# Optimization experiments

Hardware: AMD Instinct MI355X
Metric: run time of the kernel (lower is better)

Reference implementation:

```python
import jax, jax.numpy as jnp
import numpy as np

DIM = 1024
DFF = 4096
LN_EPS = 1e-5


def _layernorm(x, g, b):
    mu = jnp.mean(x, axis=-1, keepdims=True)
    var = jnp.mean((x - mu) ** 2, axis=-1, keepdims=True)
    return (x - mu) * jax.lax.rsqrt(var + LN_EPS) * g + b


def setup_inputs() -> dict:
    key = jax.random.key(0)
    ks = jax.random.split(key, 16)
    B, L, D, F = 4, 2048, DIM, DFF
    return {
        "x": jax.random.normal(ks[0], (B, L, D), dtype=jnp.float32),
        "hidden_real": jax.random.normal(ks[1], (B, D), dtype=jnp.float32),
        "hidden_imag": jax.random.normal(ks[2], (B, D), dtype=jnp.float32),
        # SConvLayer params (real/imag pairs, mirroring torch.view_as_real storage)
        "phazor_init": jax.random.normal(ks[3], (D, 2), dtype=jnp.float32),
        "phazor": jax.random.normal(ks[4], (D, 2), dtype=jnp.float32),
        # fc (gate) linear
        "fc_w": jax.random.normal(ks[5], (D, D), dtype=jnp.float32) / np.sqrt(D),
        "fc_b": jax.random.normal(ks[6], (D,), dtype=jnp.float32) * 0.01,
        # FFN
        "w1": jax.random.normal(ks[7], (F, D), dtype=jnp.float32) / np.sqrt(D),
        "b1": jax.random.normal(ks[8], (F,), dtype=jnp.float32) * 0.01,
        "w2": jax.random.normal(ks[9], (D, F), dtype=jnp.float32) / np.sqrt(F),
        "b2": jax.random.normal(ks[10], (D,), dtype=jnp.float32) * 0.01,
        # shared LayerNorm (used twice in the block with the same params)
        "ln_g": jnp.ones((D,), dtype=jnp.float32),
        "ln_b": jnp.zeros((D,), dtype=jnp.float32),
    }


def reference(x, hidden_real, hidden_imag, phazor_init, phazor,
              fc_w, fc_b, w1, b1, w2, b2, ln_g, ln_b):
    B, L, D = x.shape
    hidden = (hidden_real + 1j * hidden_imag).astype(jnp.complex64)

    x_res = x
    xn = _layernorm(x, ln_g, ln_b)

    # --- SConvLayer ---
    pz = (phazor[:, 0] + 1j * phazor[:, 1]).astype(jnp.complex64)  # [D]
    # magnitude exp(-|z|^2), phase = angle(z)
    p = jnp.exp(-(pz.real ** 2 + pz.imag ** 2)) * jnp.exp(1j * jnp.angle(pz))
    t = jnp.arange(L)
    prog = p[None, :] ** t[:, None]                      # [L, D] complex
    init_c = (phazor_init[:, 0] + 1j * phazor_init[:, 1]).astype(jnp.complex64)
    filt = prog * init_c[None, :]                        # [L, D]
    n2 = 2 * L
    filt_fft = jnp.fft.fft(filt, n=n2, axis=0)           # [2L, D]
    x_fft = jnp.fft.fft(xn.astype(jnp.complex64), n=n2, axis=1)  # [B, 2L, D]
    conv = jnp.fft.ifft(filt_fft[None] * x_fft, axis=1)[:, :L]   # [B, L, D]
    conv_with_past = conv + hidden[:, None, :] * prog[None] * p[None, None, :]
    sx = conv_with_past.real

    # --- gate ---
    y = jax.nn.silu(jnp.einsum('bld,ed->ble', x_res, fc_w) + fc_b)
    x2 = sx * y + x_res

    # --- FFN (same LayerNorm params) ---
    x3 = _layernorm(x2, ln_g, ln_b)
    h = jax.nn.silu(jnp.einsum('bld,fd->blf', x3, w1) + b1)
    out = jnp.einsum('blf,df->bld', h, w2) + b2 + x2
    return out, conv_with_past
```

## Files before the change

### kernel.cpp

```cpp
#include <hip/hip_runtime.h>
#include <hip/hip_bf16.h>

#define D_MODEL 1024
#define D_FF    4096
#define SEQ_LEN 2048
#define NBATCH  4
#define NROWS   (NBATCH*SEQ_LEN)
#define NCHUNK  32
#define CHUNK_L (SEQ_LEN/NCHUNK)
#define LN_EPS  1e-5f

typedef __hip_bfloat16 bf16;
typedef __attribute__((ext_vector_type(8))) short bf16x8;
typedef __attribute__((ext_vector_type(4))) float f32x4;

__device__ __forceinline__ void gload16(const bf16* g, bf16* l) {
    __builtin_amdgcn_global_load_lds(
        (const __attribute__((address_space(1))) void*)g,
        (__attribute__((address_space(3))) void*)l, 16, 0, 0);
}

__global__ void cast4(const float4* __restrict__ in, ushort4* __restrict__ out, int n4) {
    int i = blockIdx.x * blockDim.x + threadIdx.x;
    if (i < n4) {
        float4 v = in[i];
        union { ushort4 u; bf16 b[4]; } cv;
        cv.b[0] = __float2bfloat16(v.x); cv.b[1] = __float2bfloat16(v.y);
        cv.b[2] = __float2bfloat16(v.z); cv.b[3] = __float2bfloat16(v.w);
        out[i] = cv.u;
    }
}

__global__ void compute_pvec(const float* __restrict__ phz, float* __restrict__ pv) {
    int d = blockIdx.x * blockDim.x + threadIdx.x;
    if (d >= D_MODEL) return;
    float re = phz[2*d], im = phz[2*d+1];
    float r2 = re*re + im*im;
    float mag = expf(-r2);
    float pr, pim;
    if (r2 > 0.f) { float inv = mag / sqrtf(r2); pr = re*inv; pim = im*inv; }
    else          { pr = mag; pim = 0.f; }
    float ar = pr, ai = pim;
    #pragma unroll
    for (int i = 0; i < 6; i++) { float nr = ar*ar - ai*ai; float ni = 2.f*ar*ai; ar = nr; ai = ni; }
    pv[d]            = pr;
    pv[D_MODEL+d]    = pim;
    pv[2*D_MODEL+d]  = ar;
    pv[3*D_MODEL+d]  = ai;
}

__global__ __launch_bounds__(256) void ln_fused(const float* __restrict__ x,
                                                const float* __restrict__ g,
                                                const float* __restrict__ bta,
                                                float* __restrict__ outf,
                                                bf16*  __restrict__ outb,
                                                bf16*  __restrict__ rawb)
{
    int row = blockIdx.x;
    int tid = threadIdx.x;
    const float4* xr = (const float4*)(x + (size_t)row * D_MODEL);
    float4 v = xr[tid];
    if (rawb) {
        union { ushort4 u; bf16 b[4]; } cv;
        cv.b[0]=__float2bfloat16(v.x); cv.b[1]=__float2bfloat16(v.y);
        cv.b[2]=__float2bfloat16(v.z); cv.b[3]=__float2bfloat16(v.w);
        ((ushort4*)(rawb + (size_t)row * D_MODEL))[tid] = cv.u;
    }
    float s  = v.x + v.y + v.z + v.w;
    float s2 = v.x*v.x + v.y*v.y + v.z*v.z + v.w*v.w;
    for (int off = 32; off; off >>= 1) { s += __shfl_down(s, off); s2 += __shfl_down(s2, off); }
    __shared__ float red[8];
    int wid = tid >> 6, lane = tid & 63;
    if (lane == 0) { red[wid] = s; red[4+wid] = s2; }
    __syncthreads();
    if (tid == 0) {
        red[0] = red[0]+red[1]+red[2]+red[3];
        red[4] = red[4]+red[5]+red[6]+red[7];
    }
    __syncthreads();
    float mu  = red[0] * (1.f/D_MODEL);
    float var = red[4] * (1.f/D_MODEL) - mu*mu;
    float rstd = rsqrtf(var + LN_EPS);
    float4 gv = ((const float4*)g)[tid];
    float4 bv = ((const float4*)bta)[tid];
    float4 o;
    o.x = (v.x-mu)*rstd*gv.x + bv.x;
    o.y = (v.y-mu)*rstd*gv.y + bv.y;
    o.z = (v.z-mu)*rstd*gv.z + bv.z;
    o.w = (v.w-mu)*rstd*gv.w + bv.w;
    if (outf) ((float4*)(outf + (size_t)row * D_MODEL))[tid] = o;
    if (outb) {
        union { ushort4 u; bf16 b[4]; } cv;
        cv.b[0]=__float2bfloat16(o.x); cv.b[1]=__float2bfloat16(o.y);
        cv.b[2]=__float2bfloat16(o.z); cv.b[3]=__float2bfloat16(o.w);
        ((ushort4*)(outb + (size_t)row * D_MODEL))[tid] = cv.u;
    }
}

__global__ __launch_bounds__(256) void scan_pass1(const float* __restrict__ xn,
                                                  const float* __restrict__ pv,
                                                  const float* __restrict__ pini,
                                                  float* __restrict__ Sc)
{
    int d = blockIdx.x * 256 + threadIdx.x;
    int c = blockIdx.y, b = blockIdx.z;
    float pr = pv[d], pim = pv[D_MODEL+d];
    float icr = pini[2*d], ici = pini[2*d+1];
    float Sr = 0.f, Si = 0.f;
    const float* xp = xn + ((size_t)b*SEQ_LEN + c*CHUNK_L) * D_MODEL + d;
    #pragma unroll 8
    for (int i = 0; i < CHUNK_L; i++) {
        float xv = xp[(size_t)i * D_MODEL];
        float nr = pr*Sr - pim*Si + icr*xv;
        float ni = pr*Si + pim*Sr + ici*xv;
        Sr = nr; Si = ni;
    }
    size_t o = ((size_t)b*NCHUNK + c) * D_MODEL + d;
    Sc[2*o] = Sr; Sc[2*o+1] = Si;
}

__global__ __launch_bounds__(256) void scan_prefix(const float* __restrict__ Sc,
                                                   const float* __restrict__ pv,
                                                   const float* __restrict__ hr,
                                                   const float* __restrict__ hi,
                                                   float* __restrict__ pref)
{
    int d = blockIdx.x * 256 + threadIdx.x;
    int b = blockIdx.y;
    float qr = pv[2*D_MODEL+d], qi = pv[3*D_MODEL+d];
    float Ur = hr[b*D_MODEL+d], Ui = hi[b*D_MODEL+d];
    for (int c = 0; c < NCHUNK; c++) {
        size_t o = ((size_t)b*NCHUNK + c) * D_MODEL + d;
        pref[2*o] = Ur; pref[2*o+1] = Ui;
        float sr = Sc[2*o], si = Sc[2*o+1];
        float nr = qr*Ur - qi*Ui + sr;
        float ni = qr*Ui + qi*Ur + si;
        Ur = nr; Ui = ni;
    }
}

__global__ __launch_bounds__(256) void scan_pass2(const float* __restrict__ xn,
                                                  const float* __restrict__ pv,
                                                  const float* __restrict__ pini,
                                                  const float* __restrict__ pref,
                                                  float* __restrict__ cwp,
                                                  int interleaved)
{
    int d = blockIdx.x * 256 + threadIdx.x;
    int c = blockIdx.y, b = blockIdx.z;
    float pr = pv[d], pim = pv[D_MODEL+d];
    float icr = pini[2*d], ici = pini[2*d+1];
    size_t po = ((size_t)b*NCHUNK + c) * D_MODEL + d;
    float Ur = pref[2*po], Ui = pref[2*po+1];
    size_t base = ((size_t)b*SEQ_LEN + c*CHUNK_L) * D_MODEL + d;
    const float* xp = xn + base;
    if (interleaved) {
        float2* cp = (float2*)cwp + base;
        #pragma unroll 8
        for (int i = 0; i < CHUNK_L; i++) {
            float xv = xp[(size_t)i * D_MODEL];
            float nr = pr*Ur - pim*Ui + icr*xv;
            float ni = pr*Ui + pim*Ur + ici*xv;
            Ur = nr; Ui = ni;
            cp[(size_t)i * D_MODEL] = make_float2(Ur, Ui);
        }
    } else {
        float* cp = cwp + base;
        #pragma unroll 8
        for (int i = 0; i < CHUNK_L; i++) {
            float xv = xp[(size_t)i * D_MODEL];
            float nr = pr*Ur - pim*Ui + icr*xv;
            float ni = pr*Ui + pim*Ur + ici*xv;
            Ur = nr; Ui = ni;
            cp[(size_t)i * D_MODEL] = Ur;
        }
    }
}

#define BM 128
#define BN 128
#define BK 32

template<int EPI>
__global__ __launch_bounds__(256) void gemm_bt(const bf16* __restrict__ A,
                                               const bf16* __restrict__ Bt,
                                               const float* __restrict__ bias,
                                               const float* __restrict__ e0, int e0_stride,
                                               const float* __restrict__ e1,
                                               float* __restrict__ outf,
                                               bf16*  __restrict__ outb,
                                               int M, int N, int K)
{
    __shared__ __align__(16) bf16 As[BM*BK];
    __shared__ __align__(16) bf16 Bs[BN*BK];
    int tid = threadIdx.x;
    int m0 = blockIdx.x * BM;
    int n0 = blockIdx.y * BN;
    int wid = tid >> 6, lane = tid & 63;
    int wm = (wid >> 1) * 64, wn = (wid & 1) * 64;
    int lr = lane & 15;
    int lkc = lane >> 4;

    int rl = lane >> 2;
    int cS = (lane & 3) ^ ((rl >> 1) & 3);
    const bf16* gA0 = A  + (size_t)(m0 +      wid*16 + rl) * K + cS*8;
    const bf16* gA1 = A  + (size_t)(m0 + 64 + wid*16 + rl) * K + cS*8;
    const bf16* gB0 = Bt + (size_t)(n0 +      wid*16 + rl) * K + cS*8;
    const bf16* gB1 = Bt + (size_t)(n0 + 64 + wid*16 + rl) * K + cS*8;
    bf16* lA0 = &As[(     wid*16) * BK];
    bf16* lA1 = &As[(64 + wid*16) * BK];
    bf16* lB0 = &Bs[(     wid*16) * BK];
    bf16* lB1 = &Bs[(64 + wid*16) * BK];

    int keyr = (lr >> 1) & 3;
    int cR = (lkc ^ keyr) * 8;
    int offA[4], offB[4];
    #pragma unroll
    for (int i = 0; i < 4; i++) {
        offA[i] = (wm + i*16 + lr) * BK + cR;
        offB[i] = (wn + i*16 + lr) * BK + cR;
    }

    f32x4 acc[4][4] = {};
    for (int k0 = 0; k0 < K; k0 += BK) {
        __syncthreads();
        gload16(gA0 + k0, lA0);
        gload16(gA1 + k0, lA1);
        gload16(gB0 + k0, lB0);
        gload16(gB1 + k0, lB1);
        __syncthreads();
        bf16x8 af[4], bfv[4];
        #pragma unroll
        for (int i = 0; i < 4; i++) {
            af[i]  = *(const bf16x8*)&As[offA[i]];
            bfv[i] = *(const bf16x8*)&Bs[offB[i]];
        }
        #pragma unroll
        for (int i = 0; i < 4; i++)
            #pragma unroll
            for (int j = 0; j < 4; j++)
                acc[i][j] = __builtin_amdgcn_mfma_f32_16x16x32_bf16(af[i], bfv[j], acc[i][j], 0, 0, 0);
    }

    int mrow = 4 * (lane >> 4);
    #pragma unroll
    for (int i = 0; i < 4; i++) {
        #pragma unroll
        for (int j = 0; j < 4; j++) {
            int nb = n0 + wn + j*16 + lr;
            float bb = bias[nb];
            #pragma unroll
            for (int r = 0; r < 4; r++) {
                int m = m0 + wm + i*16 + mrow + r;
                size_t idx = (size_t)m * N + nb;
                float v = acc[i][j][r] + bb;
                if (EPI == 0) {
                    float yv = v / (1.f + __expf(-v));
                    float sxv = e0[idx * (size_t)e0_stride];
                    outf[idx] = sxv * yv + e1[idx];
                } else if (EPI == 1) {
                    float yv = v / (1.f + __expf(-v));
                    outb[idx] = __float2bfloat16(yv);
                } else {
                    outf[idx] = v + e0[idx];
                }
            }
        }
    }
}

extern "C" void kernel_launch(void* const* d_in, const int* in_sizes, int n_in,
                              void* d_out, int out_size, void* d_ws, size_t ws_size,
                              hipStream_t stream)
{
    const float* x    = (const float*)d_in[0];
    const float* hr   = (const float*)d_in[1];
    const float* hi   = (const float*)d_in[2];
    const float* pini = (const float*)d_in[3];
    const float* phz  = (const float*)d_in[4];
    const float* fcw  = (const float*)d_in[5];
    const float* fcb  = (const float*)d_in[6];
    const float* w1   = (const float*)d_in[7];
    const float* b1   = (const float*)d_in[8];
    const float* w2   = (const float*)d_in[9];
    const float* b2   = (const float*)d_in[10];
    const float* lng  = (const float*)d_in[11];
    const float* lnb  = (const float*)d_in[12];

    float* out = (float*)d_out;
    float* cwp = out + (size_t)NROWS * D_MODEL;
    int interleaved = (out_size >= NROWS * D_MODEL * 3) ? 1 : 0;

    char* ws = (char*)d_ws;
    size_t off = 0;
    bf16*  wfcb = (bf16*)(ws + off);  off += (size_t)D_MODEL*D_MODEL*2;
    bf16*  w1b  = (bf16*)(ws + off);  off += (size_t)D_FF*D_MODEL*2;
    bf16*  w2b  = (bf16*)(ws + off);  off += (size_t)D_MODEL*D_FF*2;
    float* pv   = (float*)(ws + off); off += (size_t)4*D_MODEL*4;
    float* xn   = (float*)(ws + off); off += (size_t)NROWS*D_MODEL*4;
    bf16*  xbf  = (bf16*)(ws + off);  off += (size_t)NROWS*D_MODEL*2;
    float* Sc   = (float*)(ws + off); off += (size_t)NBATCH*NCHUNK*D_MODEL*2*4;
    float* pref = (float*)(ws + off); off += (size_t)NBATCH*NCHUNK*D_MODEL*2*4;
    float* x2   = (float*)(ws + off); off += (size_t)NROWS*D_MODEL*4;
    bf16*  x3b  = (bf16*)(ws + off);  off += (size_t)NROWS*D_MODEL*2;
    bf16*  hbuf = (bf16*)(ws + off);  off += (size_t)NROWS*D_FF*2;

    cast4<<<1024, 256, 0, stream>>>((const float4*)fcw, (ushort4*)wfcb, D_MODEL*D_MODEL/4);
    cast4<<<4096, 256, 0, stream>>>((const float4*)w1,  (ushort4*)w1b,  D_FF*D_MODEL/4);
    cast4<<<4096, 256, 0, stream>>>((const float4*)w2,  (ushort4*)w2b,  D_MODEL*D_FF/4);

    compute_pvec<<<4, 256, 0, stream>>>(phz, pv);

    ln_fused<<<NROWS, 256, 0, stream>>>(x, lng, lnb, xn, nullptr, xbf);

    scan_pass1<<<dim3(4, NCHUNK, NBATCH), 256, 0, stream>>>(xn, pv, pini, Sc);
    scan_prefix<<<dim3(4, NBATCH), 256, 0, stream>>>(Sc, pv, hr, hi, pref);
    scan_pass2<<<dim3(4, NCHUNK, NBATCH), 256, 0, stream>>>(xn, pv, pini, pref, cwp, interleaved);

    gemm_bt<0><<<dim3(NROWS/BM, D_MODEL/BN), 256, 0, stream>>>(
        xbf, wfcb, fcb, cwp, interleaved ? 2 : 1, x, x2, nullptr, NROWS, D_MODEL, D_MODEL);

    ln_fused<<<NROWS, 256, 0, stream>>>(x2, lng, lnb, nullptr, x3b, nullptr);

    gemm_bt<1><<<dim3(NROWS/BM, D_FF/BN), 256, 0, stream>>>(
        x3b, w1b, b1, nullptr, 1, nullptr, nullptr, hbuf, NROWS, D_FF, D_MODEL);

    gemm_bt<2><<<dim3(NROWS/BM, D_MODEL/BN), 256, 0, stream>>>(
        hbuf, w2b, b2, x2, 1, nullptr, out, nullptr, NROWS, D_MODEL, D_FF);
}
```

Measured before the change: 324.2 us.

## Triple-buffer GEMM shared-memory tiles with async prefetch and swizzled block order

```diff
diff --git a/kernel.cpp b/kernel.cpp
--- a/kernel.cpp
+++ b/kernel.cpp
@@ -191,11 +191,17 @@
                                                bf16*  __restrict__ outb,
                                                int M, int N, int K)
 {
-    __shared__ __align__(16) bf16 As[BM*BK];
-    __shared__ __align__(16) bf16 Bs[BN*BK];
+    __shared__ __align__(16) bf16 As[3][BM*BK];
+    __shared__ __align__(16) bf16 Bs[3][BM*BK];
     int tid = threadIdx.x;
-    int m0 = blockIdx.x * BM;
-    int n0 = blockIdx.y * BN;
+
+    int nwg = gridDim.x * gridDim.y;
+    int id  = blockIdx.x + gridDim.x * blockIdx.y;
+    int cpx = nwg >> 3;
+    int sw  = (id & 7) * cpx + (id >> 3);
+    int m0  = (sw % gridDim.x) * BM;
+    int n0  = (sw / gridDim.x) * BN;
+
     int wid = tid >> 6, lane = tid & 63;
     int wm = (wid >> 1) * 64, wn = (wid & 1) * 64;
     int lr = lane & 15;
@@ -207,10 +213,8 @@
     const bf16* gA1 = A  + (size_t)(m0 + 64 + wid*16 + rl) * K + cS*8;
     const bf16* gB0 = Bt + (size_t)(n0 +      wid*16 + rl) * K + cS*8;
     const bf16* gB1 = Bt + (size_t)(n0 + 64 + wid*16 + rl) * K + cS*8;
-    bf16* lA0 = &As[(     wid*16) * BK];
-    bf16* lA1 = &As[(64 + wid*16) * BK];
-    bf16* lB0 = &Bs[(     wid*16) * BK];
-    bf16* lB1 = &Bs[(64 + wid*16) * BK];
+    int lo0 = (     wid*16) * BK;
+    int lo1 = (64 + wid*16) * BK;
 
     int keyr = (lr >> 1) & 3;
     int cR = (lkc ^ keyr) * 8;
@@ -221,26 +225,40 @@
         offB[i] = (wn + i*16 + lr) * BK + cR;
     }
 
+    int nt = K / BK;
+    auto stage = [&](int slot, int tile) {
+        int k0 = tile * BK;
+        gload16(gA0 + k0, &As[slot][lo0]);
+        gload16(gA1 + k0, &As[slot][lo1]);
+        gload16(gB0 + k0, &Bs[slot][lo0]);
+        gload16(gB1 + k0, &Bs[slot][lo1]);
+    };
+    stage(0, 0); stage(1, 1); stage(2, 2);
+
     f32x4 acc[4][4] = {};
-    for (int k0 = 0; k0 < K; k0 += BK) {
-        __syncthreads();
-        gload16(gA0 + k0, lA0);
-        gload16(gA1 + k0, lA1);
-        gload16(gB0 + k0, lB0);
-        gload16(gB1 + k0, lB1);
-        __syncthreads();
+    int s = 0;
+    for (int t = 0; t < nt; ++t) {
+        asm volatile("s_waitcnt vmcnt(8)" ::: "memory");
+        __builtin_amdgcn_s_barrier();
+        __builtin_amdgcn_sched_barrier(0);
         bf16x8 af[4], bfv[4];
         #pragma unroll
         for (int i = 0; i < 4; i++) {
-            af[i]  = *(const bf16x8*)&As[offA[i]];
-            bfv[i] = *(const bf16x8*)&Bs[offB[i]];
+            af[i]  = *(const bf16x8*)&As[s][offA[i]];
+            bfv[i] = *(const bf16x8*)&Bs[s][offB[i]];
         }
         #pragma unroll
         for (int i = 0; i < 4; i++)
             #pragma unroll
             for (int j = 0; j < 4; j++)
                 acc[i][j] = __builtin_amdgcn_mfma_f32_16x16x32_bf16(af[i], bfv[j], acc[i][j], 0, 0, 0);
-    }
+        asm volatile("" ::: "memory");
+        __builtin_amdgcn_s_barrier();
+        int nxt = t + 3; if (nxt >= nt) nxt -= nt;
+        stage(s, nxt);
+        s = (s == 2) ? 0 : s + 1;
+    }
+    asm volatile("s_waitcnt vmcnt(0)" ::: "memory");
 
     int mrow = 4 * (lane >> 4);
     #pragma unroll
```

Result: faster. 316.2 us (-2.5%).
